# Kernel optimization log

Measured on AMD Instinct MI355X. Metric: run time of the kernel, lower is better.

The kernel has to match this reference:

```python
import jax, jax.numpy as jnp
import numpy as np

B, S, D, H = 4, 1024, 1024, 16
HD = D // H


def setup_inputs() -> dict:
    key = jax.random.key(0)
    ks = jax.random.split(key, 12)
    s = 1.0 / np.sqrt(D)
    inp = {
        'q': jax.random.normal(ks[0], (B, S, D), jnp.float32),
        'k': jax.random.normal(ks[1], (B, S, D), jnp.float32),
        'v': jax.random.normal(ks[2], (B, S, D), jnp.float32),
        'mask': jnp.broadcast_to(jnp.tril(jnp.ones((S, S), jnp.int32)), (B, S, S)),
        'Wq': jax.random.uniform(ks[3], (D, D), jnp.float32, -s, s),
        'bq': jax.random.uniform(ks[4], (D,), jnp.float32, -s, s),
        'Wk': jax.random.uniform(ks[5], (D, D), jnp.float32, -s, s),
        'bk': jax.random.uniform(ks[6], (D,), jnp.float32, -s, s),
        'Wv': jax.random.uniform(ks[7], (D, D), jnp.float32, -s, s),
        'bv': jax.random.uniform(ks[8], (D,), jnp.float32, -s, s),
        'Wo': jax.random.uniform(ks[9], (D, D), jnp.float32, -s, s),
        'bo': jax.random.uniform(ks[10], (D,), jnp.float32, -s, s),
    }
    return inp


def _split_heads(x):
    # [B,S,D] -> [B,H,S,HD]
    b, s, d = x.shape
    return x.reshape(b, s, H, HD).transpose(0, 2, 1, 3)


def reference(q, k, v, mask, Wq, bq, Wk, bk, Wv, bv, Wo, bo):
    # Linear projections (torch Linear: x @ W.T + b) followed by relu
    qh = jax.nn.relu(q @ Wq.T + bq)
    kh = jax.nn.relu(k @ Wk.T + bk)
    vh = jax.nn.relu(v @ Wv.T + bv)
    qh, kh, vh = _split_heads(qh), _split_heads(kh), _split_heads(vh)
    scores = jnp.einsum('bhqd,bhkd->bhqk', qh, kh) / jnp.sqrt(jnp.float32(HD))
    scores = jnp.where(mask[:, None, :, :] == 0, jnp.float32(-1e9), scores)
    attn = jax.nn.softmax(scores, axis=-1)
    y = jnp.einsum('bhqk,bhkd->bhqd', attn, vh)
    y = y.transpose(0, 2, 1, 3).reshape(B, S, D)  # merge heads
    return jax.nn.relu(y @ Wo.T + bo)
```

## Files before the change

kernel.cpp:

```cpp
#include <hip/hip_runtime.h>


using f16    = _Float16;
using f16x4  = __attribute__((ext_vector_type(4))) _Float16;
using f16x8  = __attribute__((ext_vector_type(8))) _Float16;
using f32x4  = __attribute__((ext_vector_type(4))) float;
using f32x16 = __attribute__((ext_vector_type(16))) float;

static constexpr int S = 1024, Dm = 1024, NH = 16, HD = 64;

#if __has_builtin(__builtin_amdgcn_mfma_f32_32x32x16_f16)
#define USE_G32 1
#define MFMA32(ACC, A_, B_) \
    (ACC) = __builtin_amdgcn_mfma_f32_32x32x16_f16((A_), (B_), (ACC), 0, 0, 0)
#else
#define USE_G32 0
#endif

#if __has_builtin(__builtin_amdgcn_mfma_f32_16x16x32_f16) && \
    __has_builtin(__builtin_amdgcn_mfma_f32_16x16x16f16)
#define USE_A16 1
#define MFMA16K32(ACC, A_, B_) \
    (ACC) = __builtin_amdgcn_mfma_f32_16x16x32_f16((A_), (B_), (ACC), 0, 0, 0)
#define MFMA16(ACC, A_, B_) \
    (ACC) = __builtin_amdgcn_mfma_f32_16x16x16f16((A_), (B_), (ACC), 0, 0, 0)
#else
#define USE_A16 0
#endif

#define LO4(v) __builtin_shufflevector((v), (v), 0, 1, 2, 3)
#define HI4(v) __builtin_shufflevector((v), (v), 4, 5, 6, 7)

__device__ __forceinline__ f16x4 cvt4(float4 a) {
    f16x4 r; r[0] = (f16)a.x; r[1] = (f16)a.y; r[2] = (f16)a.z; r[3] = (f16)a.w;
    return r;
}

__device__ __forceinline__ int pcol64(int k) {
#if USE_A16
    return ((k >> 3) & 3) * 16 + ((k >> 5) << 3) + (k & 7);
#else
    return ((k >> 2) & 3) * 16 + ((k >> 4) << 2) + (k & 3);
#endif
}

__device__ __forceinline__ int swz(int row, int col) {
    return (col & ~31) | ((((col >> 3) ^ (row >> 1)) & 3) << 3) | (col & 7);
}

__device__ __forceinline__ void store_out(void* out, int mode, int m, int n, float v) {
    const int b_ = m >> 10, s_ = m & 1023, h_ = n >> 6, hd_ = n & 63;
    const size_t idx = (mode == 0)
        ? (((size_t)(b_ * NH + h_) * S + s_) * HD + pcol64(hd_))
        : (((size_t)(b_ * NH + h_) * HD + hd_) * S + s_);
    ((f16*)out)[idx] = (f16)v;
}

#if __has_builtin(__builtin_amdgcn_global_load_lds)
#define HAS_GLL 1
#else
#define HAS_GLL 0
#endif

__device__ __forceinline__ void gll16(const void* g, void* l) {
#if HAS_GLL
    __builtin_amdgcn_global_load_lds(
        (const __attribute__((address_space(1))) void*)g,
        (__attribute__((address_space(3))) void*)l, 16, 0, 0);
#else
    *(uint4*)l = *(const uint4*)g;
#endif
}

__global__ __launch_bounds__(256)
void cvt_w(const float* __restrict__ s0, const float* __restrict__ s1,
           const float* __restrict__ s2, f16* __restrict__ dst)
{
    const int z = blockIdx.y;
    const float* src = (z == 0) ? s0 : (z == 1) ? s1 : s2;
    const int e = blockIdx.x * 256 + threadIdx.x;
    const int n = e >> 8;
    const int k = (e & 255) * 4;
    const float4 v = *(const float4*)(src + (size_t)n * Dm + k);
    *(f16x4*)(dst + (size_t)z * Dm * Dm + (size_t)n * Dm + swz(n, k)) = cvt4(v);
}

__global__ __launch_bounds__(512, 6)
void gemm_qkv(const float* __restrict__ q, const float* __restrict__ k,
              const float* __restrict__ v, const f16* __restrict__ wqkv,
              const float* __restrict__ bq, const float* __restrict__ bk,
              const float* __restrict__ bv,
              f16* __restrict__ qh, f16* __restrict__ kh, f16* __restrict__ vt)
{
    const int z = blockIdx.z;
    const float* A = (z == 0) ? q : (z == 1) ? k : v;
    const float* bias = (z == 0) ? bq : (z == 1) ? bk : bv;
    f16* out = (z == 0) ? qh : (z == 1) ? kh : vt;
    const int mode = (z == 2) ? 1 : 0;
    const f16* Wf = wqkv + (size_t)z * Dm * Dm;

    const int tid = threadIdx.x;
    const int bm = blockIdx.x, bn = blockIdx.y;
#if USE_G32
    __shared__ alignas(16) float As[2][128][32];
    __shared__ alignas(16) f16   Ws[2][128][32];

    const int lane = tid & 63, wave = tid >> 6;
    const int l31 = lane & 31, kh2 = lane >> 5;
    const int wm = wave & 3, wn = wave >> 2;

    const int arow = tid >> 3;
    const int aslotD = tid & 7;
    const int aslotS = aslotD ^ (arow & 7);
    const float* Asrc0 = A + (size_t)(bm * 128 + arow) * Dm + aslotS * 4;
    const int wrow = tid >> 2, wcol = (tid & 3) * 8;
    const f16* Wsrc0 = Wf + (size_t)(bn * 128 + wrow) * Dm + wcol;

    auto dma = [&](int k0, int buf) {
        gll16(Asrc0 + k0,                      &As[buf][arow][aslotD * 4]);
        gll16(Asrc0 + (size_t)64 * Dm + k0,    &As[buf][64 + arow][aslotD * 4]);
        gll16(Wsrc0 + k0,                      &Ws[buf][wrow][wcol]);
    };

    auto afrag = [&](int buf, int r, int s) -> f16x8 {
        const int p = s * 4 + kh2 * 2, r7 = r & 7;
        const f32x4 lo = *(const f32x4*)&As[buf][r][(p ^ r7) * 4];
        const f32x4 hi = *(const f32x4*)&As[buf][r][((p + 1) ^ r7) * 4];
        f16x8 f;
        f[0] = (f16)lo[0]; f[1] = (f16)lo[1]; f[2] = (f16)lo[2]; f[3] = (f16)lo[3];
        f[4] = (f16)hi[0]; f[5] = (f16)hi[1]; f[6] = (f16)hi[2]; f[7] = (f16)hi[3];
        return f;
    };
    auto wfrag = [&](int buf, int r, int s) -> f16x8 {
        const int sl = s * 2 + kh2;
        return *(const f16x8*)&Ws[buf][r][((sl ^ (r >> 1)) & 3) * 8];
    };

    f32x16 acc[2] = {};
    auto kslice = [&](int buf, int s) {
        const f16x8 af  = afrag(buf, wm * 32 + l31, s);
        const f16x8 bf0 = wfrag(buf, wn * 64 + l31, s);
        const f16x8 bf1 = wfrag(buf, wn * 64 + 32 + l31, s);
        MFMA32(acc[0], af, bf0);
        MFMA32(acc[1], af, bf1);
    };

    constexpr int NIT = Dm / 32;
    dma(0, 0);
    for (int t = 0; t < NIT; ++t) {
        const int cur = t & 1;
        __syncthreads();
        if (t + 1 < NIT) dma((t + 1) * 32, cur ^ 1);
        kslice(cur, 0);
        kslice(cur, 1);
    }

#pragma unroll
    for (int j = 0; j < 2; ++j) {
        const int col = bn * 128 + wn * 64 + j * 32 + l31;
        const float bb = bias[col];
#pragma unroll
        for (int blk = 0; blk < 4; ++blk) {
            const int row0 = bm * 128 + wm * 32 + 8 * blk + 4 * kh2;
            if (mode == 1) {
                const int b_ = row0 >> 10, s_ = row0 & 1023;
                const int h_ = col >> 6, hd_ = col & 63;
                f16x4 vv;
#pragma unroll
                for (int r = 0; r < 4; ++r)
                    vv[r] = (f16)fmaxf(acc[j][blk * 4 + r] + bb, 0.0f);
                *(f16x4*)&out[((size_t)(b_ * NH + h_) * HD + hd_) * S + s_] = vv;
            } else {
#pragma unroll
                for (int r = 0; r < 4; ++r)
                    store_out(out, mode, row0 + r, col,
                              fmaxf(acc[j][blk * 4 + r] + bb, 0.0f));
            }
        }
    }
#else
    for (int i = tid; i < 128 * 128; i += 512) {
        const int m = bm * 128 + (i >> 7);
        const int n = bn * 128 + (i & 127);
        float acc = 0.0f;
        for (int k2 = 0; k2 < Dm; ++k2)
            acc = fmaf(A[(size_t)m * Dm + k2], (float)Wf[(size_t)n * Dm + swz(n, k2)], acc);
        store_out(out, mode, m, n, fmaxf(acc + bias[n], 0.0f));
    }
#endif
}

__global__ __launch_bounds__(256, 6)
void gemm_out(const f16* __restrict__ y, const float* __restrict__ wo,
              const float* __restrict__ bo, float* __restrict__ out)
{
    const int tid = threadIdx.x;
    const int bm = blockIdx.x, bn = blockIdx.y;
#if USE_G32
    __shared__ alignas(16) f16   As[2][64][32];
    __shared__ alignas(16) float Wsf[2][64][32];

    const int lane = tid & 63, wave = tid >> 6;
    const int l31 = lane & 31, kh2 = lane >> 5;
    const int wm = wave & 1, wn = wave >> 1;

    const int drow = tid >> 2, dcol = (tid & 3) * 8;
    const f16* Asrc = y + (size_t)(bm * 64 + drow) * Dm + dcol;
    const int wrow = tid >> 3;
    const int wslotD = tid & 7;
    const int wslotS = wslotD ^ (wrow & 7);
    const float* Wsrc0 = wo + (size_t)(bn * 64 + wrow) * Dm + wslotS * 4;

    auto dma = [&](int k0, int buf) {
        gll16(Asrc + k0, &As[buf][drow][dcol]);
        gll16(Wsrc0 + k0,                   &Wsf[buf][wrow][wslotD * 4]);
        gll16(Wsrc0 + (size_t)32 * Dm + k0, &Wsf[buf][32 + wrow][wslotD * 4]);
    };
    auto yfrag = [&](int buf, int r, int s) -> f16x8 {
        const int sl = s * 2 + kh2;
        return *(const f16x8*)&As[buf][r][((sl ^ (r >> 1)) & 3) * 8];
    };
    auto wfrag32 = [&](int buf, int r, int s) -> f16x8 {
        const int p = s * 4 + kh2 * 2, r7 = r & 7;
        const f32x4 lo = *(const f32x4*)&Wsf[buf][r][(p ^ r7) * 4];
        const f32x4 hi = *(const f32x4*)&Wsf[buf][r][((p + 1) ^ r7) * 4];
        f16x8 f;
        f[0] = (f16)lo[0]; f[1] = (f16)lo[1]; f[2] = (f16)lo[2]; f[3] = (f16)lo[3];
        f[4] = (f16)hi[0]; f[5] = (f16)hi[1]; f[6] = (f16)hi[2]; f[7] = (f16)hi[3];
        return f;
    };

    f32x16 acc = {};
    constexpr int NIT = Dm / 32;
    dma(0, 0);
    for (int t = 0; t < NIT; ++t) {
        const int cur = t & 1;
        __syncthreads();
        if (t + 1 < NIT) dma((t + 1) * 32, cur ^ 1);
#pragma unroll
        for (int s = 0; s < 2; ++s) {
            const f16x8 af = yfrag(cur, wm * 32 + l31, s);
            const f16x8 bf = wfrag32(cur, wn * 32 + l31, s);
            MFMA32(acc, af, bf);
        }
    }

    const int col = bn * 64 + wn * 32 + l31;
    const float bb = bo[col];
#pragma unroll
    for (int blk = 0; blk < 4; ++blk) {
        const int row0 = bm * 64 + wm * 32 + 8 * blk + 4 * kh2;
#pragma unroll
        for (int r = 0; r < 4; ++r)
            out[(size_t)(row0 + r) * Dm + col] = fmaxf(acc[blk * 4 + r] + bb, 0.0f);
    }
#else
    for (int i = tid; i < 64 * 64; i += 256) {
        const int m = bm * 64 + (i >> 6);
        const int n = bn * 64 + (i & 63);
        float acc = 0.0f;
        for (int k2 = 0; k2 < Dm; ++k2)
            acc = fmaf((float)y[(size_t)m * Dm + swz(m, k2)],
                       wo[(size_t)n * Dm + k2], acc);
        out[(size_t)m * Dm + n] = fmaxf(acc + bo[n], 0.0f);
    }
#endif
}

__global__ __launch_bounds__(256)
void attn_fwd(const f16* __restrict__ qh, const f16* __restrict__ kh,
              const f16* __restrict__ vt, f16* __restrict__ y)
{
    const int bz = blockIdx.x;
    const int qt = bz & 15;
    const int h  = (bz >> 4) & 15;
    const int b  = bz >> 8;
    const size_t head = (size_t)(b * NH + h) * S * HD;

#if USE_A16
    __shared__ alignas(16) f16 Ks[2][64][72];
    __shared__ alignas(16) f16 Vs[2][64][72];

    const int tid  = threadIdx.x;
    const int wave = tid >> 6;
    const int lane = tid & 63;
    const int l15  = lane & 15;
    const int quad = lane >> 4;
    const int sr   = tid >> 2;
    const int sc   = (tid & 3) * 16;

    const f16* Qrow = qh + head + (size_t)(qt * 64 + wave * 16 + l15) * HD;
    const f16* Kp   = kh + head;
    const f16* Vp   = vt + head;

    f16x8 aq[2];
    {
        const uint4 q0 = *(const uint4*)(Qrow + quad * 16);
        const uint4 q1 = *(const uint4*)(Qrow + quad * 16 + 8);
        aq[0] = *(f16x8*)&q0;
        aq[1] = *(f16x8*)&q1;
    }

    const int qg = qt * 64 + wave * 16 + l15;
    float m_i = -1e30f, l_i = 0.0f;
    f32x4 acc_o[4] = {};

    uint4 pk[2], pv[2];
    auto pref = [&](int kt) {
        const f16* Kr = Kp + (size_t)(kt * 64 + sr) * HD + sc;
        pk[0] = *(const uint4*)Kr;
        pk[1] = *(const uint4*)(Kr + 8);
        const f16* Vr = Vp + (size_t)sr * S + kt * 64 + sc;
        pv[0] = *(const uint4*)Vr;
        pv[1] = *(const uint4*)(Vr + 8);
    };

    pref(0);
    for (int kt = 0; kt <= qt; ++kt) {
        const int cur = kt & 1;
        *(uint4*)&Ks[cur][sr][sc]     = pk[0];
        *(uint4*)&Ks[cur][sr][sc + 8] = pk[1];
        {
            const int sb = (sc >> 4) * 4;
            *(f16x4*)&Vs[cur][sr][0 * 16 + sb] = *(f16x4*)((f16*)&pv[0]);
            *(f16x4*)&Vs[cur][sr][1 * 16 + sb] = *(f16x4*)((f16*)&pv[0] + 4);
            *(f16x4*)&Vs[cur][sr][2 * 16 + sb] = *(f16x4*)((f16*)&pv[1]);
            *(f16x4*)&Vs[cur][sr][3 * 16 + sb] = *(f16x4*)((f16*)&pv[1] + 4);
        }
        __syncthreads();
        if (kt < qt) pref(kt + 1);

        f32x4 accs[4] = {};
#pragma unroll
        for (int t = 0; t < 4; ++t) {
            const f16x8 k8a = *(const f16x8*)&Ks[cur][t * 16 + l15][quad * 16];
            const f16x8 k8b = *(const f16x8*)&Ks[cur][t * 16 + l15][quad * 16 + 8];
            MFMA16K32(accs[t], k8a, aq[0]);
            MFMA16K32(accs[t], k8b, aq[1]);
        }

        const int key0 = kt * 64 + quad * 4;
#pragma unroll
        for (int t = 0; t < 4; ++t)
#pragma unroll
            for (int r = 0; r < 4; ++r) {
                float sv = accs[t][r] * 0.125f;
                if (key0 + t * 16 + r > qg) sv = -1e9f;
                accs[t][r] = sv;
            }

        float mx = accs[0][0];
#pragma unroll
        for (int t = 0; t < 4; ++t)
#pragma unroll
            for (int r = 0; r < 4; ++r) mx = fmaxf(mx, accs[t][r]);
        mx = fmaxf(mx, __shfl_xor(mx, 16, 64));
        mx = fmaxf(mx, __shfl_xor(mx, 32, 64));
        const float mnew = fmaxf(m_i, mx);
        float sm = 0.0f;
#pragma unroll
        for (int t = 0; t < 4; ++t)
#pragma unroll
            for (int r = 0; r < 4; ++r) {
                const float e = __expf(accs[t][r] - mnew);
                accs[t][r] = e;
                sm += e;
            }
        sm += __shfl_xor(sm, 16, 64);
        sm += __shfl_xor(sm, 32, 64);
        const float alpha = __expf(m_i - mnew);
        l_i = l_i * alpha + sm;
        m_i = mnew;

        f16x4 ap[4];
#pragma unroll
        for (int c = 0; c < 4; ++c) {
            f16x4 v;
#pragma unroll
            for (int j = 0; j < 4; ++j) v[j] = (f16)accs[c][j];
            ap[c] = v;
        }

        float ar[4];
#pragma unroll
        for (int r = 0; r < 4; ++r) ar[r] = __shfl(alpha, quad * 4 + r, 64);
#pragma unroll
        for (int t2 = 0; t2 < 4; ++t2)
#pragma unroll
            for (int r = 0; r < 4; ++r) acc_o[t2][r] *= ar[r];
#pragma unroll
        for (int t2 = 0; t2 < 4; ++t2) {
            const f16x8 v8a = *(const f16x8*)&Vs[cur][t2 * 16 + l15][quad * 16];
            const f16x8 v8b = *(const f16x8*)&Vs[cur][t2 * 16 + l15][quad * 16 + 8];
            MFMA16(acc_o[t2], ap[0], LO4(v8a));
            MFMA16(acc_o[t2], ap[1], HI4(v8a));
            MFMA16(acc_o[t2], ap[2], LO4(v8b));
            MFMA16(acc_o[t2], ap[3], HI4(v8b));
        }
    }

    float lr[4];
#pragma unroll
    for (int r = 0; r < 4; ++r) lr[r] = __shfl(l_i, quad * 4 + r, 64);
#pragma unroll
    for (int t2 = 0; t2 < 4; ++t2)
#pragma unroll
        for (int r = 0; r < 4; ++r) {
            const int srow = qt * 64 + wave * 16 + quad * 4 + r;
            const int dcol = h * 64 + t2 * 16 + l15;
            y[((size_t)b * S + srow) * Dm + swz(srow, dcol)] =
                (f16)(acc_o[t2][r] / lr[r]);
        }
#else
    const int tid = threadIdx.x;
    if (tid < 64) {
        const int q = qt * 64 + tid;
        const f16* Qr = qh + head + (size_t)q * HD;
        float qv[64];
        for (int d = 0; d < 64; ++d) qv[d] = (float)Qr[pcol64(d)];
        float mx = -1e30f;
        for (int key = 0; key <= q; ++key) {
            const f16* Kr = kh + head + (size_t)key * HD;
            float s = 0.0f;
            for (int d = 0; d < 64; ++d) s = fmaf(qv[d], (float)Kr[pcol64(d)], s);
            mx = fmaxf(mx, s * 0.125f);
        }
        float o[64];
        for (int d = 0; d < 64; ++d) o[d] = 0.0f;
        float l = 0.0f;
        for (int key = 0; key <= q; ++key) {
            const f16* Kr = kh + head + (size_t)key * HD;
            float s = 0.0f;
            for (int d = 0; d < 64; ++d) s = fmaf(qv[d], (float)Kr[pcol64(d)], s);
            const float p = __expf(s * 0.125f - mx);
            l += p;
            for (int d = 0; d < 64; ++d)
                o[d] = fmaf(p, (float)vt[head + (size_t)d * S + key], o[d]);
        }
        for (int d = 0; d < 64; ++d)
            y[((size_t)b * S + q) * Dm + swz(q, h * 64 + d)] = (f16)(o[d] / l);
    }
#endif
}

extern "C" void kernel_launch(void* const* d_in, const int* in_sizes, int n_in,
                              void* d_out, int out_size, void* d_ws, size_t ws_size,
                              hipStream_t stream)
{
    f16* ws = (f16*)d_ws;
    const size_t SEG = (size_t)4 * 1024 * 1024;
    f16* qh   = ws;
    f16* kh   = ws + SEG;
    f16* vt   = ws + 2 * SEG;
    f16* wqkv = ws + 3 * SEG;
    f16* y    = ws + 3 * SEG;

    cvt_w<<<dim3(1024, 3), 256, 0, stream>>>(
        (const float*)d_in[4], (const float*)d_in[6], (const float*)d_in[8], wqkv);
    gemm_qkv<<<dim3(32, 8, 3), 512, 0, stream>>>(
        (const float*)d_in[0], (const float*)d_in[1], (const float*)d_in[2],
        wqkv,
        (const float*)d_in[5], (const float*)d_in[7], (const float*)d_in[9],
        qh, kh, vt);
    attn_fwd<<<dim3(4 * NH * (S / 64)), 256, 0, stream>>>(qh, kh, vt, y);
    gemm_out<<<dim3(64, 16), 256, 0, stream>>>(
        y, (const float*)d_in[10], (const float*)d_in[11], (float*)d_out);
}
```

Measured before the change: 251.2 us.

## Enlarge attention query tile to 128 rows with 512-thread blocks sharing K/V

The attention kernel now gives each block 128 query rows handled by 8 waves instead of 64 rows by 4 waves, so each K/V tile staged in shared memory serves twice as many queries. The global staging loads are rewritten so each thread loads one 16-byte K chunk and one V chunk, keeping the same permuted V layout. The aim is to halve K/V global traffic and per-query staging overhead. In exchange the lower half of each block computes one fully masked causal tile, and the grid shrinks to half as many, larger blocks, which can hurt load balance across CUs.

```diff
diff --git a/kernel.cpp b/kernel.cpp
--- a/kernel.cpp
+++ b/kernel.cpp
@@ -267,14 +267,14 @@
 #endif
 }
 
-__global__ __launch_bounds__(256)
+__global__ __launch_bounds__(512, 6)
 void attn_fwd(const f16* __restrict__ qh, const f16* __restrict__ kh,
               const f16* __restrict__ vt, f16* __restrict__ y)
 {
     const int bz = blockIdx.x;
-    const int qt = bz & 15;
-    const int h  = (bz >> 4) & 15;
-    const int b  = bz >> 8;
+    const int qt = bz & 7;
+    const int h  = (bz >> 3) & 15;
+    const int b  = bz >> 7;
     const size_t head = (size_t)(b * NH + h) * S * HD;
 
 #if USE_A16
@@ -286,10 +286,10 @@
     const int lane = tid & 63;
     const int l15  = lane & 15;
     const int quad = lane >> 4;
-    const int sr   = tid >> 2;
-    const int sc   = (tid & 3) * 16;
-
-    const f16* Qrow = qh + head + (size_t)(qt * 64 + wave * 16 + l15) * HD;
+    const int sr   = tid >> 3;
+    const int t8   = tid & 7;
+
+    const f16* Qrow = qh + head + (size_t)(qt * 128 + wave * 16 + l15) * HD;
     const f16* Kp   = kh + head;
     const f16* Vp   = vt + head;
 
@@ -301,34 +301,31 @@
         aq[1] = *(f16x8*)&q1;
     }
 
-    const int qg = qt * 64 + wave * 16 + l15;
+    const int qg = qt * 128 + wave * 16 + l15;
     float m_i = -1e30f, l_i = 0.0f;
     f32x4 acc_o[4] = {};
 
-    uint4 pk[2], pv[2];
+    const int vc0 = 16 * ((2 * t8) & 3) + 4 * (t8 >> 1);
+    const int vc1 = 16 * ((2 * t8 + 1) & 3) + 4 * (t8 >> 1);
+
+    uint4 pk, pv;
     auto pref = [&](int kt) {
-        const f16* Kr = Kp + (size_t)(kt * 64 + sr) * HD + sc;
-        pk[0] = *(const uint4*)Kr;
-        pk[1] = *(const uint4*)(Kr + 8);
-        const f16* Vr = Vp + (size_t)sr * S + kt * 64 + sc;
-        pv[0] = *(const uint4*)Vr;
-        pv[1] = *(const uint4*)(Vr + 8);
-    };
-
+        pk = *(const uint4*)(Kp + (size_t)(kt * 64 + sr) * HD + t8 * 8);
+        pv = *(const uint4*)(Vp + (size_t)sr * S + kt * 64 + t8 * 8);
+    };
+
+    const int ktmax = 2 * qt + 1;
     pref(0);
-    for (int kt = 0; kt <= qt; ++kt) {
+    for (int kt = 0; kt <= ktmax; ++kt) {
         const int cur = kt & 1;
-        *(uint4*)&Ks[cur][sr][sc]     = pk[0];
-        *(uint4*)&Ks[cur][sr][sc + 8] = pk[1];
+        *(uint4*)&Ks[cur][sr][t8 * 8] = pk;
         {
-            const int sb = (sc >> 4) * 4;
-            *(f16x4*)&Vs[cur][sr][0 * 16 + sb] = *(f16x4*)((f16*)&pv[0]);
-            *(f16x4*)&Vs[cur][sr][1 * 16 + sb] = *(f16x4*)((f16*)&pv[0] + 4);
-            *(f16x4*)&Vs[cur][sr][2 * 16 + sb] = *(f16x4*)((f16*)&pv[1]);
-            *(f16x4*)&Vs[cur][sr][3 * 16 + sb] = *(f16x4*)((f16*)&pv[1] + 4);
+            f16x8 pv8 = *(f16x8*)&pv;
+            *(f16x4*)&Vs[cur][sr][vc0] = LO4(pv8);
+            *(f16x4*)&Vs[cur][sr][vc1] = HI4(pv8);
         }
         __syncthreads();
-        if (kt < qt) pref(kt + 1);
+        if (kt < ktmax) pref(kt + 1);
 
         f32x4 accs[4] = {};
 #pragma unroll
@@ -406,15 +403,15 @@
     for (int t2 = 0; t2 < 4; ++t2)
 #pragma unroll
         for (int r = 0; r < 4; ++r) {
-            const int srow = qt * 64 + wave * 16 + quad * 4 + r;
+            const int srow = qt * 128 + wave * 16 + quad * 4 + r;
             const int dcol = h * 64 + t2 * 16 + l15;
             y[((size_t)b * S + srow) * Dm + swz(srow, dcol)] =
                 (f16)(acc_o[t2][r] / lr[r]);
         }
 #else
     const int tid = threadIdx.x;
-    if (tid < 64) {
-        const int q = qt * 64 + tid;
+    if (tid < 128) {
+        const int q = qt * 128 + tid;
         const f16* Qr = qh + head + (size_t)q * HD;
         float qv[64];
         for (int d = 0; d < 64; ++d) qv[d] = (float)Qr[pcol64(d)];
@@ -462,7 +459,7 @@
         wqkv,
         (const float*)d_in[5], (const float*)d_in[7], (const float*)d_in[9],
         qh, kh, vt);
-    attn_fwd<<<dim3(4 * NH * (S / 64)), 256, 0, stream>>>(qh, kh, vt, y);
+    attn_fwd<<<dim3(4 * NH * (S / 128)), 512, 0, stream>>>(qh, kh, vt, y);
     gemm_out<<<dim3(64, 16), 256, 0, stream>>>(
         y, (const float*)d_in[10], (const float*)d_in[11], (float*)d_out);
 }
```

New measurement: 238.7 us. -5.0%, faster.
